# Optimization experiments

Measured on AMD Instinct MI355X. Metric: run time of the kernel, lower is better.

Reference implementation:

```python
import jax, jax.numpy as jnp
import numpy as np


def setup_inputs() -> dict:
    key = jax.random.key(0)
    k1, k2, k3, k4 = jax.random.split(key, 4)
    B, T, C, H = 32, 2048, 384, 64
    x = jax.random.normal(k1, (B, T, C), dtype=jnp.float32)
    # nn.Linear(C, H, bias=False): weight stored [H, C], applied as x @ W.T.
    # We store the transposed [C, H] form directly.
    s = 1.0 / np.sqrt(C)
    Wk = jax.random.normal(k2, (C, H), dtype=jnp.float32) * s
    Wq = jax.random.normal(k3, (C, H), dtype=jnp.float32) * s
    Wv = jax.random.normal(k4, (C, H), dtype=jnp.float32) * s
    return {"x": x, "Wk": Wk, "Wq": Wq, "Wv": Wv}


def reference(x, Wk, Wq, Wv):
    # x: [B, T, C]; Wk/Wq/Wv: [C, H]
    T = x.shape[1]
    H = Wk.shape[1]
    k = jnp.einsum('btc,ch->bth', x, Wk)
    q = jnp.einsum('btc,ch->bth', x, Wq)
    v = jnp.einsum('btc,ch->bth', x, Wv)
    scale = H ** (-0.5)
    scores = jnp.einsum('bth,bsh->bts', q, k) * scale  # [B, T, T]
    causal = jnp.tril(jnp.ones((T, T), dtype=bool))
    scores = jnp.where(causal, scores, -jnp.inf)
    attn = jax.nn.softmax(scores, axis=-1)
    # dropout is identity in eval mode
    out = jnp.einsum('bts,bsh->bth', attn, v)  # [B, T, H]
    return out
```

## Files before the change

kernel.cpp:

```cpp
#include <hip/hip_runtime.h>

typedef __bf16 bf16_8 __attribute__((ext_vector_type(8)));
typedef __bf16 bf16_4 __attribute__((ext_vector_type(4)));
typedef float  f32x4  __attribute__((ext_vector_type(4)));

#define NB 32
#define NT 2048
#define NC 384
#define NH 64

static __device__ __forceinline__ f32x4 mfma16(bf16_8 a, bf16_8 b, f32x4 c) {
  return __builtin_amdgcn_mfma_f32_16x16x32_bf16(a, b, c, 0, 0, 0);
}

__global__ void pack_w_kernel(const float* __restrict__ Wk, const float* __restrict__ Wq,
                              const float* __restrict__ Wv, __bf16* __restrict__ Wt) {
  int idx = blockIdx.x * 256 + threadIdx.x;
  if (idx >= 192 * NC) return;
  int n = idx / NC, k = idx % NC;
  int sel = n >> 6, h = n & 63;
  const float* W = (sel == 0) ? Wq : (sel == 1 ? Wk : Wv);
  float v = W[k * NH + h];
  if (sel == 0) v *= 0.125f * 1.44269504088896340736f;
  Wt[idx] = (__bf16)v;
}

__launch_bounds__(1024, 4)
__global__ void qkv_kernel(const float* __restrict__ x, const __bf16* __restrict__ Wt,
                           __bf16* __restrict__ Q, __bf16* __restrict__ K,
                           __bf16* __restrict__ Vt) {
  __shared__ __bf16 Wl[192 * 384];

  const int tid  = threadIdx.x;
  const int lane = tid & 63, wq = tid >> 6;
  const int quad = lane >> 4, l16 = lane & 15;
  const int rowblk = blockIdx.x * 256;
  const int rbase  = rowblk + wq * 16;
  const int row    = rbase + l16;

  #pragma unroll
  for (int i = 0; i < 9; ++i) {
    int g = tid + i * 1024;
    int r = g / 48, c = g - r * 48;
    int p = c ^ (r & 7);
    uint4 v = ((const uint4*)Wt)[g];
    *(uint4*)&Wl[(r * 48 + p) * 8] = v;
  }
  __syncthreads();

  f32x4 acc[12];
  #pragma unroll
  for (int n = 0; n < 12; ++n) acc[n] = f32x4{0.f, 0.f, 0.f, 0.f};

  const float* xrow = x + (size_t)row * NC;
  f32x4 x0 = *(const f32x4*)(xrow + quad * 8);
  f32x4 x1 = *(const f32x4*)(xrow + quad * 8 + 4);

  #pragma unroll
  for (int kc = 0; kc < 12; ++kc) {
    f32x4 nx0, nx1;
    if (kc < 11) {
      const float* xp = xrow + (kc + 1) * 32 + quad * 8;
      nx0 = *(const f32x4*)xp;
      nx1 = *(const f32x4*)(xp + 4);
    }
    bf16_8 a;
    a[0] = (__bf16)x0[0]; a[1] = (__bf16)x0[1]; a[2] = (__bf16)x0[2]; a[3] = (__bf16)x0[3];
    a[4] = (__bf16)x1[0]; a[5] = (__bf16)x1[1]; a[6] = (__bf16)x1[2]; a[7] = (__bf16)x1[3];
    const int pc = (kc * 4 + quad) ^ (l16 & 7);
    const int cbase = l16 * 48 + pc;
    #pragma unroll
    for (int n = 0; n < 12; ++n) {
      bf16_8 b = *(const bf16_8*)&Wl[(n * 16 * 48 + cbase) * 8];
      acc[n] = mfma16(a, b, acc[n]);
    }
    x0 = nx0; x1 = nx1;
  }

  __syncthreads();
  __bf16 (*Qs)[72]  = (__bf16(*)[72])Wl;
  __bf16 (*Ks2)[72] = (__bf16(*)[72])(Wl + 18432);
  __bf16 (*Vl)[264] = (__bf16(*)[264])(Wl + 36864);

  #pragma unroll
  for (int n = 0; n < 4; ++n)
    #pragma unroll
    for (int r = 0; r < 4; ++r) {
      int t = wq * 16 + quad * 4 + r;
      int h = n * 16 + l16;
      Qs[t][h]  = (__bf16)acc[n][r];
      Ks2[t][h] = (__bf16)acc[n + 4][r];
    }
  #pragma unroll
  for (int n = 8; n < 12; ++n) {
    int h = (n - 8) * 16 + l16;
    int t0 = wq * 16 + quad * 4;
    bf16_4 p;
    p[0] = (__bf16)acc[n][0]; p[1] = (__bf16)acc[n][1];
    p[2] = (__bf16)acc[n][2]; p[3] = (__bf16)acc[n][3];
    *(bf16_4*)&Vl[h][t0] = p;
  }
  __syncthreads();

  {
    int t = tid >> 2, h0 = (tid & 3) * 16;
    __bf16* qdst = Q + (size_t)(rowblk + t) * NH + h0;
    __bf16* kdst = K + (size_t)(rowblk + t) * NH + h0;
    const __bf16* qsrc = &Qs[t][h0];
    const __bf16* ksrc = &Ks2[t][h0];
    ((uint4*)qdst)[0] = ((const uint4*)qsrc)[0];
    ((uint4*)qdst)[1] = ((const uint4*)qsrc)[1];
    ((uint4*)kdst)[0] = ((const uint4*)ksrc)[0];
    ((uint4*)kdst)[1] = ((const uint4*)ksrc)[1];
  }
  {
    int h = tid >> 4, seg = tid & 15;
    int bb = rowblk >> 11, t0 = (rowblk & (NT - 1)) + seg * 16;
    const __bf16* src = &Vl[h][seg * 16];
    __bf16* dst = Vt + ((size_t)(bb * NH + h)) * NT + t0;
    ((uint4*)dst)[0] = ((const uint4*)src)[0];
    ((uint4*)dst)[1] = ((const uint4*)src)[1];
  }
}

__launch_bounds__(256)
__global__ void attn_kernel(const __bf16* __restrict__ Q, const __bf16* __restrict__ K,
                            const __bf16* __restrict__ Vt, float* __restrict__ out) {
  __shared__ __bf16 Ks[2][64][72];
  __shared__ __bf16 Vs[2][64][72];

  const int tid  = threadIdx.x;
  const int lane = tid & 63, wq = tid >> 6;
  const int quad = lane >> 4, l16 = lane & 15;
  const int b    = blockIdx.x >> 4;
  const int pair = blockIdx.x & 15;

  const float NEG_INF = -__builtin_inff();
  const float RTHR = 8.f;
  const int r = tid >> 2, seg = tid & 3;
  const __bf16* Kg = K  + (size_t)b * NT * NH;
  const __bf16* Vg = Vt + (size_t)b * NH * NT;

  const int c0 = seg * 4;
  const int kp0 = ((c0 & 8) << 2) + ((c0 & 3) << 3) + (((c0 >> 2) & 1) << 2);
  const int kp1 = (((c0+1) & 8) << 2) + (((c0+1) & 3) << 3) + ((((c0+1) >> 2) & 1) << 2);
  const int kp2 = (((c0+2) & 8) << 2) + (((c0+2) & 3) << 3) + ((((c0+2) >> 2) & 1) << 2);
  const int kp3 = (((c0+3) & 8) << 2) + (((c0+3) & 3) << 3) + ((((c0+3) >> 2) & 1) << 2);

  for (int pass = 0; pass < 2; ++pass) {
    const int qt = pass ? pair : (31 - pair);
    const int q0 = qt * 64;
    const int nIter = qt + 1;

    const __bf16* qrow = Q + ((size_t)(b * NT + q0 + wq * 16 + l16)) * NH + quad * 8;
    bf16_8 qf0 = *(const bf16_8*)qrow;
    bf16_8 qf1 = *(const bf16_8*)(qrow + 32);

    f32x4 o[4];
    #pragma unroll
    for (int i = 0; i < 4; ++i) o[i] = f32x4{0.f, 0.f, 0.f, 0.f};
    float m_i = NEG_INF, l_i = 0.f;

    __syncthreads();

    {
      const uint4* sK = (const uint4*)(Kg + (size_t)r * NH + seg * 16);
      uint4 ka = sK[0], kb = sK[1];
      const uint4* sV = (const uint4*)(Vg + (size_t)r * NT + seg * 16);
      uint4 va = sV[0], vb = sV[1];
      *(uint4*)&Ks[0][r][seg * 16]     = ka;
      *(uint4*)&Ks[0][r][seg * 16 + 8] = kb;
      *(uint2*)&Vs[0][r][kp0] = make_uint2(va.x, va.y);
      *(uint2*)&Vs[0][r][kp1] = make_uint2(va.z, va.w);
      *(uint2*)&Vs[0][r][kp2] = make_uint2(vb.x, vb.y);
      *(uint2*)&Vs[0][r][kp3] = make_uint2(vb.z, vb.w);
    }

    for (int i = 0; i < nIter; ++i) {
      const int cur = i & 1;
      const bool more = (i + 1 < nIter);
      uint4 nka, nkb, nva, nvb;
      if (more) {
        const int s0n = (i + 1) * 64;
        const uint4* sK = (const uint4*)(Kg + (size_t)(s0n + r) * NH + seg * 16);
        nka = sK[0]; nkb = sK[1];
        const uint4* sV = (const uint4*)(Vg + (size_t)r * NT + s0n + seg * 16);
        nva = sV[0]; nvb = sV[1];
      }
      __syncthreads();

      f32x4 s[4];
      __builtin_amdgcn_s_setprio(1);
      #pragma unroll
      for (int st = 0; st < 4; ++st) {
        bf16_8 a0 = *(const bf16_8*)&Ks[cur][st * 16 + l16][quad * 8];
        bf16_8 a1 = *(const bf16_8*)&Ks[cur][st * 16 + l16][quad * 8 + 32];
        f32x4 accv = f32x4{0.f, 0.f, 0.f, 0.f};
        accv = mfma16(a0, qf0, accv);
        accv = mfma16(a1, qf1, accv);
        s[st] = accv;
      }
      __builtin_amdgcn_s_setprio(0);

      if (i == qt) {
        int qg = wq * 16 + l16;
        #pragma unroll
        for (int st = 0; st < 4; ++st)
          #pragma unroll
          for (int rr = 0; rr < 4; ++rr) {
            int sg = st * 16 + quad * 4 + rr;
            if (sg > qg) s[st][rr] = NEG_INF;
          }
      }

      float mx = NEG_INF;
      #pragma unroll
      for (int st = 0; st < 4; ++st)
        #pragma unroll
        for (int rr = 0; rr < 4; ++rr) mx = fmaxf(mx, s[st][rr]);
      mx = fmaxf(mx, __shfl_xor(mx, 16));
      mx = fmaxf(mx, __shfl_xor(mx, 32));

      float m_new = fmaxf(m_i, mx);
      if (__any(m_new - m_i > RTHR)) {
        float alpha = exp2f(m_i - m_new);
        f32x4 av;
        #pragma unroll
        for (int rr = 0; rr < 4; ++rr) av[rr] = __shfl(alpha, quad * 4 + rr);
        #pragma unroll
        for (int nt = 0; nt < 4; ++nt)
          #pragma unroll
          for (int rr = 0; rr < 4; ++rr) o[nt][rr] *= av[rr];
        l_i *= alpha;
        m_i = m_new;
      }

      float lsum = 0.f;
      bf16_8 pa0, pa1;
      #pragma unroll
      for (int st = 0; st < 4; ++st)
        #pragma unroll
        for (int rr = 0; rr < 4; ++rr) {
          float p = exp2f(s[st][rr] - m_i);
          lsum += p;
          __bf16 pb = (__bf16)p;
          if (st < 2) pa0[st * 4 + rr] = pb;
          else        pa1[(st - 2) * 4 + rr] = pb;
        }
      lsum += __shfl_xor(lsum, 16);
      lsum += __shfl_xor(lsum, 32);
      l_i += lsum;

      __builtin_amdgcn_s_setprio(1);
      #pragma unroll
      for (int nt = 0; nt < 4; ++nt) {
        bf16_8 b0 = *(const bf16_8*)&Vs[cur][nt * 16 + l16][quad * 8];
        bf16_8 b1 = *(const bf16_8*)&Vs[cur][nt * 16 + l16][quad * 8 + 32];
        o[nt] = mfma16(pa0, b0, o[nt]);
        o[nt] = mfma16(pa1, b1, o[nt]);
      }
      __builtin_amdgcn_s_setprio(0);

      if (more) {
        *(uint4*)&Ks[1 - cur][r][seg * 16]     = nka;
        *(uint4*)&Ks[1 - cur][r][seg * 16 + 8] = nkb;
        *(uint2*)&Vs[1 - cur][r][kp0] = make_uint2(nva.x, nva.y);
        *(uint2*)&Vs[1 - cur][r][kp1] = make_uint2(nva.z, nva.w);
        *(uint2*)&Vs[1 - cur][r][kp2] = make_uint2(nvb.x, nvb.y);
        *(uint2*)&Vs[1 - cur][r][kp3] = make_uint2(nvb.z, nvb.w);
      }
    }

    f32x4 lv;
    #pragma unroll
    for (int rr = 0; rr < 4; ++rr) lv[rr] = 1.f / __shfl(l_i, quad * 4 + rr);
    float* op = out + ((size_t)(b * NT + q0 + wq * 16 + quad * 4)) * NH + l16;
    #pragma unroll
    for (int nt = 0; nt < 4; ++nt)
      #pragma unroll
      for (int rr = 0; rr < 4; ++rr)
        op[(size_t)rr * NH + nt * 16] = o[nt][rr] * lv[rr];
  }
}

extern "C" void kernel_launch(void* const* d_in, const int* in_sizes, int n_in,
                              void* d_out, int out_size, void* d_ws, size_t ws_size,
                              hipStream_t stream) {
  const float* x  = (const float*)d_in[0];
  const float* Wk = (const float*)d_in[1];
  const float* Wq = (const float*)d_in[2];
  const float* Wv = (const float*)d_in[3];
  float* out = (float*)d_out;

  char* ws = (char*)d_ws;
  __bf16* Wt  = (__bf16*)ws;
  __bf16* Qb  = (__bf16*)(ws + 256 * 1024);
  __bf16* Kb  = Qb + (size_t)NB * NT * NH;
  __bf16* Vtb = Kb + (size_t)NB * NT * NH;

  pack_w_kernel<<<288, 256, 0, stream>>>(Wk, Wq, Wv, Wt);
  qkv_kernel<<<256, 1024, 0, stream>>>(x, Wt, Qb, Kb, Vtb);
  attn_kernel<<<NB * 16, 256, 0, stream>>>(Qb, Kb, Vtb, out);
}
```

Baseline: 207.3 us.

## Split long causal query tiles across two blocks with split-KV and a merge kernel

The attention grid doubles from 512 to 1024 blocks. For each paired long query tile, one block handles KV tiles 0-15 and another handles the rest plus the short paired tile, so each block carries about 16 tiles of work. Partial outputs with their running max and sum go to a workspace buffer, and a new merge kernel combines them with log-sum-exp rescaling. The aim is more parallelism and better CU occupancy, helped by a launch bound asking for 4 blocks per CU. The cost is an extra kernel launch and the partial-buffer traffic.

```diff
diff --git a/kernel.cpp b/kernel.cpp
--- a/kernel.cpp
+++ b/kernel.cpp
@@ -123,17 +123,20 @@
   }
 }
 
-__launch_bounds__(256)
+__launch_bounds__(256, 4)
 __global__ void attn_kernel(const __bf16* __restrict__ Q, const __bf16* __restrict__ K,
-                            const __bf16* __restrict__ Vt, float* __restrict__ out) {
+                            const __bf16* __restrict__ Vt, float* __restrict__ out,
+                            float* __restrict__ Part) {
   __shared__ __bf16 Ks[2][64][72];
   __shared__ __bf16 Vs[2][64][72];
 
   const int tid  = threadIdx.x;
   const int lane = tid & 63, wq = tid >> 6;
   const int quad = lane >> 4, l16 = lane & 15;
-  const int b    = blockIdx.x >> 4;
-  const int pair = blockIdx.x & 15;
+  const int b    = blockIdx.x >> 5;
+  const int u    = blockIdx.x & 31;
+  const int side = u >> 4, pair = u & 15;
+  const int qt_hi = 31 - pair;
 
   const float NEG_INF = -__builtin_inff();
   const float RTHR = 8.f;
@@ -147,10 +150,13 @@
   const int kp2 = (((c0+2) & 8) << 2) + (((c0+2) & 3) << 3) + ((((c0+2) >> 2) & 1) << 2);
   const int kp3 = (((c0+3) & 8) << 2) + (((c0+3) & 3) << 3) + ((((c0+3) >> 2) & 1) << 2);
 
-  for (int pass = 0; pass < 2; ++pass) {
-    const int qt = pass ? pair : (31 - pair);
+  const int nseg = side ? 2 : 1;
+  for (int sg = 0; sg < nseg; ++sg) {
+    int qt, s0, s1, partial;
+    if (side == 0)      { qt = qt_hi; s0 = 0;  s1 = 16;        partial = 1; }
+    else if (sg == 0)   { qt = qt_hi; s0 = 16; s1 = qt_hi + 1; partial = 1; }
+    else                { qt = pair;  s0 = 0;  s1 = pair + 1;  partial = 0; }
     const int q0 = qt * 64;
-    const int nIter = qt + 1;
 
     const __bf16* qrow = Q + ((size_t)(b * NT + q0 + wq * 16 + l16)) * NH + quad * 8;
     bf16_8 qf0 = *(const bf16_8*)qrow;
@@ -164,9 +170,9 @@
     __syncthreads();
 
     {
-      const uint4* sK = (const uint4*)(Kg + (size_t)r * NH + seg * 16);
+      const uint4* sK = (const uint4*)(Kg + (size_t)(s0 * 64 + r) * NH + seg * 16);
       uint4 ka = sK[0], kb = sK[1];
-      const uint4* sV = (const uint4*)(Vg + (size_t)r * NT + seg * 16);
+      const uint4* sV = (const uint4*)(Vg + (size_t)r * NT + s0 * 64 + seg * 16);
       uint4 va = sV[0], vb = sV[1];
       *(uint4*)&Ks[0][r][seg * 16]     = ka;
       *(uint4*)&Ks[0][r][seg * 16 + 8] = kb;
@@ -176,9 +182,9 @@
       *(uint2*)&Vs[0][r][kp3] = make_uint2(vb.z, vb.w);
     }
 
-    for (int i = 0; i < nIter; ++i) {
-      const int cur = i & 1;
-      const bool more = (i + 1 < nIter);
+    for (int i = s0; i < s1; ++i) {
+      const int cur = (i - s0) & 1;
+      const bool more = (i + 1 < s1);
       uint4 nka, nkb, nva, nvb;
       if (more) {
         const int s0n = (i + 1) * 64;
@@ -208,8 +214,8 @@
         for (int st = 0; st < 4; ++st)
           #pragma unroll
           for (int rr = 0; rr < 4; ++rr) {
-            int sg = st * 16 + quad * 4 + rr;
-            if (sg > qg) s[st][rr] = NEG_INF;
+            int sg2 = st * 16 + quad * 4 + rr;
+            if (sg2 > qg) s[st][rr] = NEG_INF;
           }
       }
 
@@ -271,15 +277,56 @@
       }
     }
 
-    f32x4 lv;
+    if (partial) {
+      float* slot = Part + ((size_t)((b * 16 + pair) * 2 + (side ? 1 : 0))) * 4224;
+      #pragma unroll
+      for (int nt = 0; nt < 4; ++nt)
+        #pragma unroll
+        for (int rr = 0; rr < 4; ++rr)
+          slot[(wq * 16 + quad * 4 + rr) * 64 + nt * 16 + l16] = o[nt][rr];
+      if (quad == 0) {
+        slot[4096 + wq * 16 + l16] = m_i;
+        slot[4160 + wq * 16 + l16] = l_i;
+      }
+    } else {
+      f32x4 lv;
+      #pragma unroll
+      for (int rr = 0; rr < 4; ++rr) lv[rr] = 1.f / __shfl(l_i, quad * 4 + rr);
+      float* op = out + ((size_t)(b * NT + q0 + wq * 16 + quad * 4)) * NH + l16;
+      #pragma unroll
+      for (int nt = 0; nt < 4; ++nt)
+        #pragma unroll
+        for (int rr = 0; rr < 4; ++rr)
+          op[(size_t)rr * NH + nt * 16] = o[nt][rr] * lv[rr];
+    }
+  }
+}
+
+__global__ void merge_kernel(const float* __restrict__ Part, float* __restrict__ out) {
+  const int blk = blockIdx.x;
+  const int b = blk >> 4, pair = blk & 15;
+  const int qt_hi = 31 - pair;
+  const int t = threadIdx.x;
+  const int q = t >> 2, h0 = (t & 3) * 16;
+
+  const float* A = Part + ((size_t)((b * 16 + pair) * 2)) * 4224;
+  const float* B = A + 4224;
+  float mA = A[4096 + q], mB = B[4096 + q];
+  float lA = A[4160 + q], lB = B[4160 + q];
+  float m  = fmaxf(mA, mB);
+  float aA = exp2f(mA - m), aB = exp2f(mB - m);
+  float linv = 1.f / (lA * aA + lB * aB);
+  aA *= linv; aB *= linv;
+
+  float* op = out + ((size_t)(b * NT + qt_hi * 64 + q)) * NH + h0;
+  #pragma unroll
+  for (int j = 0; j < 16; j += 4) {
+    f32x4 oa = *(const f32x4*)&A[q * 64 + h0 + j];
+    f32x4 ob = *(const f32x4*)&B[q * 64 + h0 + j];
+    f32x4 rv;
     #pragma unroll
-    for (int rr = 0; rr < 4; ++rr) lv[rr] = 1.f / __shfl(l_i, quad * 4 + rr);
-    float* op = out + ((size_t)(b * NT + q0 + wq * 16 + quad * 4)) * NH + l16;
-    #pragma unroll
-    for (int nt = 0; nt < 4; ++nt)
-      #pragma unroll
-      for (int rr = 0; rr < 4; ++rr)
-        op[(size_t)rr * NH + nt * 16] = o[nt][rr] * lv[rr];
+    for (int rr = 0; rr < 4; ++rr) rv[rr] = oa[rr] * aA + ob[rr] * aB;
+    *(f32x4*)&op[j] = rv;
   }
 }
 
@@ -297,8 +344,10 @@
   __bf16* Qb  = (__bf16*)(ws + 256 * 1024);
   __bf16* Kb  = Qb + (size_t)NB * NT * NH;
   __bf16* Vtb = Kb + (size_t)NB * NT * NH;
+  float*  Part = (float*)(ws + (size_t)26 * 1024 * 1024);
 
   pack_w_kernel<<<288, 256, 0, stream>>>(Wk, Wq, Wv, Wt);
   qkv_kernel<<<256, 1024, 0, stream>>>(x, Wt, Qb, Kb, Vtb);
-  attn_kernel<<<NB * 16, 256, 0, stream>>>(Qb, Kb, Vtb, out);
-}
+  attn_kernel<<<NB * 32, 256, 0, stream>>>(Qb, Kb, Vtb, out, Part);
+  merge_kernel<<<NB * 16, 256, 0, stream>>>(Part, out);
+}
```

Measured after the change: 212.4 us. 2.4% more time.

## Defer P·V MFMA by one tile to overlap with next QK and softmax

Applied to the files above, without the earlier changes.

The P·V matrix multiply for tile i is moved into iteration i+1, placed right after that iteration's QK^T MFMAs, with a final drain after the loop. V shared memory becomes triple-buffered so the previous tile's V stays valid while the next one is staged. The aim is to let MFMA work overlap the exp/reduction softmax phase and hide the dependency between softmax and P·V. The cost is extra LDS (one more V buffer) and longer register live ranges for the deferred P fragments.

```diff
diff --git a/kernel.cpp b/kernel.cpp
--- a/kernel.cpp
+++ b/kernel.cpp
@@ -127,7 +127,7 @@
 __global__ void attn_kernel(const __bf16* __restrict__ Q, const __bf16* __restrict__ K,
                             const __bf16* __restrict__ Vt, float* __restrict__ out) {
   __shared__ __bf16 Ks[2][64][72];
-  __shared__ __bf16 Vs[2][64][72];
+  __shared__ __bf16 Vs[3][64][72];
 
   const int tid  = threadIdx.x;
   const int lane = tid & 63, wq = tid >> 6;
@@ -160,6 +160,7 @@
     #pragma unroll
     for (int i = 0; i < 4; ++i) o[i] = f32x4{0.f, 0.f, 0.f, 0.f};
     float m_i = NEG_INF, l_i = 0.f;
+    bf16_8 pa0, pa1;
 
     __syncthreads();
 
@@ -176,8 +177,11 @@
       *(uint2*)&Vs[0][r][kp3] = make_uint2(vb.z, vb.w);
     }
 
+    int vcur = 0;
     for (int i = 0; i < nIter; ++i) {
-      const int cur = i & 1;
+      const int kcur  = i & 1;
+      const int vprev = (vcur == 0) ? 2 : vcur - 1;
+      const int vnext = (vcur == 2) ? 0 : vcur + 1;
       const bool more = (i + 1 < nIter);
       uint4 nka, nkb, nva, nvb;
       if (more) {
@@ -193,13 +197,22 @@
       __builtin_amdgcn_s_setprio(1);
       #pragma unroll
       for (int st = 0; st < 4; ++st) {
-        bf16_8 a0 = *(const bf16_8*)&Ks[cur][st * 16 + l16][quad * 8];
-        bf16_8 a1 = *(const bf16_8*)&Ks[cur][st * 16 + l16][quad * 8 + 32];
+        bf16_8 a0 = *(const bf16_8*)&Ks[kcur][st * 16 + l16][quad * 8];
+        bf16_8 a1 = *(const bf16_8*)&Ks[kcur][st * 16 + l16][quad * 8 + 32];
         f32x4 accv = f32x4{0.f, 0.f, 0.f, 0.f};
         accv = mfma16(a0, qf0, accv);
         accv = mfma16(a1, qf1, accv);
         s[st] = accv;
       }
+      if (i > 0) {
+        #pragma unroll
+        for (int nt = 0; nt < 4; ++nt) {
+          bf16_8 b0 = *(const bf16_8*)&Vs[vprev][nt * 16 + l16][quad * 8];
+          bf16_8 b1 = *(const bf16_8*)&Vs[vprev][nt * 16 + l16][quad * 8 + 32];
+          o[nt] = mfma16(pa0, b0, o[nt]);
+          o[nt] = mfma16(pa1, b1, o[nt]);
+        }
+      }
       __builtin_amdgcn_s_setprio(0);
 
       if (i == qt) {
@@ -208,8 +221,8 @@
         for (int st = 0; st < 4; ++st)
           #pragma unroll
           for (int rr = 0; rr < 4; ++rr) {
-            int sg = st * 16 + quad * 4 + rr;
-            if (sg > qg) s[st][rr] = NEG_INF;
+            int sg2 = st * 16 + quad * 4 + rr;
+            if (sg2 > qg) s[st][rr] = NEG_INF;
           }
       }
 
@@ -236,7 +249,6 @@
       }
 
       float lsum = 0.f;
-      bf16_8 pa0, pa1;
       #pragma unroll
       for (int st = 0; st < 4; ++st)
         #pragma unroll
@@ -251,26 +263,27 @@
       lsum += __shfl_xor(lsum, 32);
       l_i += lsum;
 
-      __builtin_amdgcn_s_setprio(1);
+      if (more) {
+        *(uint4*)&Ks[1 - kcur][r][seg * 16]     = nka;
+        *(uint4*)&Ks[1 - kcur][r][seg * 16 + 8] = nkb;
+        *(uint2*)&Vs[vnext][r][kp0] = make_uint2(nva.x, nva.y);
+        *(uint2*)&Vs[vnext][r][kp1] = make_uint2(nva.z, nva.w);
+        *(uint2*)&Vs[vnext][r][kp2] = make_uint2(nvb.x, nvb.y);
+        *(uint2*)&Vs[vnext][r][kp3] = make_uint2(nvb.z, nvb.w);
+      }
+      vcur = vnext;
+    }
+
+    {
+      const int vlast = (vcur == 0) ? 2 : vcur - 1;
       #pragma unroll
       for (int nt = 0; nt < 4; ++nt) {
-        bf16_8 b0 = *(const bf16_8*)&Vs[cur][nt * 16 + l16][quad * 8];
-        bf16_8 b1 = *(const bf16_8*)&Vs[cur][nt * 16 + l16][quad * 8 + 32];
+        bf16_8 b0 = *(const bf16_8*)&Vs[vlast][nt * 16 + l16][quad * 8];
+        bf16_8 b1 = *(const bf16_8*)&Vs[vlast][nt * 16 + l16][quad * 8 + 32];
         o[nt] = mfma16(pa0, b0, o[nt]);
         o[nt] = mfma16(pa1, b1, o[nt]);
       }
-      __builtin_amdgcn_s_setprio(0);
-
-      if (more) {
-        *(uint4*)&Ks[1 - cur][r][seg * 16]     = nka;
-        *(uint4*)&Ks[1 - cur][r][seg * 16 + 8] = nkb;
-        *(uint2*)&Vs[1 - cur][r][kp0] = make_uint2(nva.x, nva.y);
-        *(uint2*)&Vs[1 - cur][r][kp1] = make_uint2(nva.z, nva.w);
-        *(uint2*)&Vs[1 - cur][r][kp2] = make_uint2(nvb.x, nvb.y);
-        *(uint2*)&Vs[1 - cur][r][kp3] = make_uint2(nvb.z, nvb.w);
-      }
-    }
-
+    }
     f32x4 lv;
     #pragma unroll
     for (int rr = 0; rr < 4; ++rr) lv[rr] = 1.f / __shfl(l_i, quad * 4 + rr);
```

New measurement: 212.1 us. +2.3%, slower.
